# Kernel tuning notes

Measured on AMD Instinct MI355X. Metric: run time of the kernel, lower is better.

## Reference

```python
import jax, jax.numpy as jnp
import numpy as np
from jax.scipy.linalg import solve_triangular

EPS = 2e-05  # module eps (original only adds it on Cholesky failure)
NUM_LABELS = 8


def setup_inputs() -> dict:
    key = jax.random.key(0)
    k1, k2, k3, k4 = jax.random.split(key, 4)
    B, N, H, W = 1, 256, 512, 512
    return {
        "content_feat": jax.random.normal(k1, (B, N, H, W), dtype=jnp.float32),
        "style_feat": jax.random.normal(k2, (B, N, H, W), dtype=jnp.float32),
        "content_seg": jax.random.randint(k3, (H, W), 0, NUM_LABELS, dtype=jnp.int32),
        "style_seg": jax.random.randint(k4, (H, W), 0, NUM_LABELS, dtype=jnp.int32),
        "num_labels": NUM_LABELS,
    }


def _cwct(c, s, seg_c, seg_s, num_labels):
    # c, s: (N, M) flattened features; seg_*: (M,) int labels
    N = c.shape[0]
    eye = jnp.eye(N, dtype=c.dtype)
    target = c
    for l in range(num_labels):  # fixed small label count
        mc = (seg_c == l)  # (Mc,) content mask
        ms = (seg_s == l)
        nc = mc.sum().astype(c.dtype)
        ns = ms.sum().astype(c.dtype)
        nc1 = jnp.maximum(nc, 1.0)
        ns1 = jnp.maximum(ns, 1.0)
        # masked mean + centered (zeros outside mask)
        mean_c = (c * mc).sum(-1) / nc1
        xc = (c - mean_c[:, None]) * mc  # (N, M)
        cov_c = (xc @ xc.T) / jnp.maximum(nc1 - 1.0, 1.0)  # (N, N)
        Lc = jnp.linalg.cholesky(cov_c)
        inv_Lc = solve_triangular(Lc, eye, lower=True)
        white = inv_Lc @ xc
        # style stats + coloring
        mean_s = (s * ms).sum(-1) / ns1
        xs = (s - mean_s[:, None]) * ms
        cov_s = (xs @ xs.T) / jnp.maximum(ns1 - 1.0, 1.0)
        Ls = jnp.linalg.cholesky(cov_s)
        colored = Ls @ white + mean_s[:, None]
        # label validity: >10 pixels each side, count ratio < 100
        valid = (nc > 10) & (ns > 10) & (nc < 100.0 * ns) & (ns < 100.0 * nc)
        target = jnp.where(mc[None, :] & valid, colored, target)
    return target


def reference(content_feat, style_feat, content_seg, style_seg, num_labels):
    B, N, cH, cW = content_feat.shape  # B == 1 (original code only supports B=1)
    c = content_feat.reshape(N, cH * cW)
    s = style_feat.reshape(N, -1)
    out = _cwct(c, s, content_seg.reshape(-1), style_seg.reshape(-1), num_labels)
    return out.reshape(B, N, cH, cW)
```

## Files before the change

kernel.cpp:

```cpp
#include <hip/hip_runtime.h>

#define NCH   256
#define M_PIX 262144
#define MPAD  266240
#define LDA   40

typedef short bf16x8 __attribute__((ext_vector_type(8)));
typedef float f32x4  __attribute__((ext_vector_type(4)));

__device__ __forceinline__ unsigned short f2bf(float f) {
  union { float f; unsigned u; } v; v.f = f;
  unsigned r = v.u + 0x7FFFu + ((v.u >> 16) & 1u);
  return (unsigned short)(r >> 16);
}
__device__ __forceinline__ float bf2f(unsigned short h) {
  union { unsigned u; float f; } v; v.u = ((unsigned)h) << 16;
  return v.f;
}

__global__ __launch_bounds__(256) void k_hist(const int* __restrict__ seg_c,
                                              const int* __restrict__ seg_s,
                                              int* __restrict__ hist) {
  __shared__ int h[16];
  int t = threadIdx.x;
  if (t < 16) h[t] = 0;
  __syncthreads();
  int p0 = blockIdx.x * 2048 + t * 8;
#pragma unroll
  for (int e = 0; e < 8; ++e) {
    atomicAdd(&h[seg_c[p0 + e] & 7], 1);
    atomicAdd(&h[8 + (seg_s[p0 + e] & 7)], 1);
  }
  __syncthreads();
  if (t < 8) hist[blockIdx.x * 8 + t] = h[t];
  else if (t < 16) hist[1024 + blockIdx.x * 8 + (t - 8)] = h[t];
}

__global__ __launch_bounds__(256) void k_scan(const int* __restrict__ hist,
                                              int* __restrict__ base,
                                              int* __restrict__ off,
                                              int* __restrict__ cnt,
                                              int* __restrict__ valid) {
  __shared__ int lh[2048];
  __shared__ int tot[16];
  __shared__ int loff[2][9];
  int t = threadIdx.x;
  for (int i = t; i < 2048; i += 256) lh[i] = hist[i];
  __syncthreads();
  if (t < 16) {
    int s = t >> 3, l = t & 7, acc = 0;
    for (int b = 0; b < 128; ++b) acc += lh[s * 1024 + b * 8 + l];
    tot[t] = acc;
  }
  __syncthreads();
  if (t < 2) {
    int run = 0;
    for (int l = 0; l < 8; ++l) {
      loff[t][l] = run;
      run = (run + tot[t * 8 + l] + 511) & ~511;
    }
    loff[t][8] = run;
    for (int l = 0; l < 9; ++l) off[t * 9 + l] = loff[t][l];
    for (int l = 0; l < 8; ++l) cnt[t * 8 + l] = tot[t * 8 + l];
  }
  __syncthreads();
  if (t < 8) {
    long nc = tot[t], ns = tot[8 + t];
    valid[t] = (nc > 10 && ns > 10 && nc < 100 * ns && ns < 100 * nc) ? 1 : 0;
  }
  if (t < 16) {
    int s = t >> 3, l = t & 7;
    int run = loff[s][l];
    for (int b = 0; b < 128; ++b) {
      base[s * 1024 + b * 8 + l] = run;
      run += lh[s * 1024 + b * 8 + l];
    }
  }
}

__global__ __launch_bounds__(256) void k_rank(const int* __restrict__ seg_c,
                                              const int* __restrict__ seg_s,
                                              const int* __restrict__ base,
                                              int* __restrict__ dst) {
  __shared__ int sc[8 * 272];
  __shared__ int rb[256 * 8];
  __shared__ int bb[8];
  int t = threadIdx.x;
  for (int s = 0; s < 2; ++s) {
    const int* seg = s ? seg_s : seg_c;
    const int* bas = base + s * 1024 + blockIdx.x * 8;
    int* dd = dst + (size_t)s * M_PIX;
    int p0 = blockIdx.x * 2048 + t * 8;
    unsigned pk2 = 0, cpk = 0;
#pragma unroll
    for (int e = 0; e < 8; ++e) {
      int lb = seg[p0 + e] & 7;
      pk2 |= (unsigned)lb << (3 * e);
      cpk += 1u << (4 * lb);
    }
#pragma unroll
    for (int lq = 0; lq < 8; ++lq) sc[lq * 272 + t] = (int)((cpk >> (4 * lq)) & 15u);
    if (t < 8) bb[t] = bas[t];
    __syncthreads();
    for (int d = 1; d < 256; d <<= 1) {
      int v[8];
#pragma unroll
      for (int lq = 0; lq < 8; ++lq)
        v[lq] = sc[lq * 272 + t] + ((t >= d) ? sc[lq * 272 + t - d] : 0);
      __syncthreads();
#pragma unroll
      for (int lq = 0; lq < 8; ++lq) sc[lq * 272 + t] = v[lq];
      __syncthreads();
    }
#pragma unroll
    for (int lq = 0; lq < 8; ++lq)
      rb[t * 8 + lq] = bb[lq] + sc[lq * 272 + t] - (int)((cpk >> (4 * lq)) & 15u);
#pragma unroll
    for (int e = 0; e < 8; ++e) {
      int lb = (int)((pk2 >> (3 * e)) & 7u);
      int dpos = rb[t * 8 + lb]++;
      dd[p0 + e] = dpos;
    }
    __syncthreads();
  }
}

__global__ __launch_bounds__(256) void k_padzero(unsigned short* __restrict__ P,
                                                 const int* __restrict__ off,
                                                 const int* __restrict__ cnt) {
  int l = blockIdx.x;
  int c0, c1;
  if (l < 8) { c0 = off[l] + cnt[l]; c1 = off[l + 1]; }
  else       { c0 = off[8];          c1 = MPAD; }
  int w = c1 - c0;
  if (w <= 0) return;
  for (int r = 0; r < 256; ++r)
    for (int cc = threadIdx.x; cc < w; cc += 256)
      P[(size_t)r * MPAD + c0 + cc] = 0;
}

__global__ __launch_bounds__(256) void k_pack(const float* __restrict__ feat,
                                              const int* __restrict__ seg,
                                              const int* __restrict__ dst,
                                              const int* __restrict__ base,
                                              unsigned short* __restrict__ P) {
  int b = blockIdx.x, g = blockIdx.y, t = threadIdx.x;
  int p0 = b * 2048;
  __shared__ unsigned short buf[8][2048];
  __shared__ int h[8], lbase[9], gbase[8];
  if (t < 8) { h[t] = 0; gbase[t] = base[b * 8 + t]; }
  __syncthreads();
  int lb[8], slot[8], gd[8];
#pragma unroll
  for (int i = 0; i < 8; ++i) {
    lb[i] = seg[p0 + i * 256 + t] & 7;
    atomicAdd(&h[lb[i]], 1);
  }
  __syncthreads();
  if (t == 0) {
    int run = 0;
    for (int l = 0; l < 8; ++l) { lbase[l] = run; run += h[l]; }
    lbase[8] = run;
  }
  __syncthreads();
#pragma unroll
  for (int i = 0; i < 8; ++i)
    slot[i] = lbase[lb[i]] + (dst[p0 + i * 256 + t] - gbase[lb[i]]);
#pragma unroll
  for (int i = 0; i < 8; ++i) {
    int q = i * 256 + t;
    int l = 0;
    while (l < 7 && q >= lbase[l + 1]) ++l;
    gd[i] = gbase[l] + q - lbase[l];
  }
  int n0 = g * 32;
#pragma unroll 1
  for (int cp = 0; cp < 4; ++cp) {
#pragma unroll
    for (int c = 0; c < 8; ++c) {
      const float* fp = &feat[(size_t)(n0 + cp * 8 + c) * M_PIX + p0];
#pragma unroll
      for (int i = 0; i < 8; ++i)
        buf[c][slot[i]] = f2bf(fp[i * 256 + t]);
    }
    __syncthreads();
#pragma unroll
    for (int c = 0; c < 8; ++c) {
      unsigned short* pp = &P[(size_t)(n0 + cp * 8 + c) * MPAD];
#pragma unroll
      for (int i = 0; i < 8; ++i)
        pp[gd[i]] = buf[c][i * 256 + t];
    }
    __syncthreads();
  }
}

__global__ __launch_bounds__(256) void k_unpack(const unsigned short* __restrict__ P,
                                                const int* __restrict__ seg,
                                                const int* __restrict__ dst,
                                                const int* __restrict__ base,
                                                float* __restrict__ out) {
  int b = blockIdx.x, g = blockIdx.y, t = threadIdx.x;
  int p0 = b * 2048;
  __shared__ unsigned short buf[8][2048];
  __shared__ int h[8], lbase[9], gbase[8];
  if (t < 8) { h[t] = 0; gbase[t] = base[b * 8 + t]; }
  __syncthreads();
  int lb[8], slot[8], gd[8];
#pragma unroll
  for (int i = 0; i < 8; ++i) {
    lb[i] = seg[p0 + i * 256 + t] & 7;
    atomicAdd(&h[lb[i]], 1);
  }
  __syncthreads();
  if (t == 0) {
    int run = 0;
    for (int l = 0; l < 8; ++l) { lbase[l] = run; run += h[l]; }
    lbase[8] = run;
  }
  __syncthreads();
#pragma unroll
  for (int i = 0; i < 8; ++i)
    slot[i] = lbase[lb[i]] + (dst[p0 + i * 256 + t] - gbase[lb[i]]);
#pragma unroll
  for (int i = 0; i < 8; ++i) {
    int q = i * 256 + t;
    int l = 0;
    while (l < 7 && q >= lbase[l + 1]) ++l;
    gd[i] = gbase[l] + q - lbase[l];
  }
  int n0 = g * 32;
#pragma unroll 1
  for (int cp = 0; cp < 4; ++cp) {
#pragma unroll
    for (int c = 0; c < 8; ++c) {
      const unsigned short* pp = &P[(size_t)(n0 + cp * 8 + c) * MPAD];
#pragma unroll
      for (int i = 0; i < 8; ++i)
        buf[c][i * 256 + t] = pp[gd[i]];
    }
    __syncthreads();
#pragma unroll
    for (int c = 0; c < 8; ++c) {
      float* op = &out[(size_t)(n0 + cp * 8 + c) * M_PIX + p0];
#pragma unroll
      for (int i = 0; i < 8; ++i)
        op[i * 256 + t] = bf2f(buf[c][slot[i]]);
    }
    __syncthreads();
  }
}

__global__ __launch_bounds__(512) void k_gram(const unsigned short* __restrict__ P,
                                              const int* __restrict__ off,
                                              float* __restrict__ G,
                                              float* __restrict__ sum) {
  int l = blockIdx.y;
  long o0 = off[l], o1 = off[l + 1];
  long k0 = o0 + (long)blockIdx.x * 1024;
  if (k0 >= o1) return;
  long rem = o1 - k0;
  int ks = rem > 1024 ? 1024 : (int)rem;

  __shared__ unsigned short Sb[256 * LDA];
  int t = threadIdx.x, wave = t >> 6, lane = t & 63;
  int wr = (wave < 2) ? wave * 64 : 128 + (wave & 1) * 64;
  int wc = (wave >= 4) ? 128 : 0;
  bool wact = (wave < 6);

  f32x4 acc[4][8] = {};
  float rsum = 0.0f;

  for (int kk = 0; kk < ks; kk += 32) {
#pragma unroll
    for (int it = 0; it < 2; ++it) {
      int slot = t + it * 512;
      int rr = slot >> 2, gg = slot & 3;
      *(uint4*)&Sb[rr * LDA + gg * 8] =
          *(const uint4*)&P[(size_t)rr * MPAD + (size_t)(k0 + kk) + gg * 8];
    }
    __syncthreads();
    if (t < 256) {
#pragma unroll
      for (int e = 0; e < 16; ++e) {
        unsigned v = *(const unsigned*)&Sb[t * LDA + e * 2];
        rsum += bf2f((unsigned short)(v & 0xFFFFu)) + bf2f((unsigned short)(v >> 16));
      }
    }
    if (wact) {
      bf16x8 bfr[8];
#pragma unroll
      for (int fj = 0; fj < 8; ++fj)
        bfr[fj] = *(const bf16x8*)&Sb[(wc + fj * 16 + (lane & 15)) * LDA + (lane >> 4) * 8];
#pragma unroll
      for (int fi = 0; fi < 4; ++fi) {
        bf16x8 afr = *(const bf16x8*)&Sb[(wr + fi * 16 + (lane & 15)) * LDA + (lane >> 4) * 8];
#pragma unroll
        for (int fj = 0; fj < 8; ++fj)
          acc[fi][fj] = __builtin_amdgcn_mfma_f32_16x16x32_bf16(afr, bfr[fj], acc[fi][fj], 0, 0, 0);
      }
    }
    __syncthreads();
  }
  float* Gl = G + ((size_t)l << 16);
  if (wact) {
#pragma unroll
    for (int fi = 0; fi < 4; ++fi)
#pragma unroll
      for (int fj = 0; fj < 8; ++fj) {
        int cc = wc + fj * 16 + (lane & 15);
#pragma unroll
        for (int rg = 0; rg < 4; ++rg) {
          int rr2 = wr + fi * 16 + (lane >> 4) * 4 + rg;
          atomicAdd(&Gl[rr2 * 256 + cc], acc[fi][fj][rg]);
        }
      }
  }
  if (t < 256) atomicAdd(&sum[l * 256 + t], rsum);
}

__global__ __launch_bounds__(256) void k_cov(float* __restrict__ G,
                                             const float* __restrict__ sum,
                                             const int* __restrict__ cnt,
                                             float* __restrict__ means) {
  int bid = blockIdx.x;
  float* A = G + ((size_t)bid << 16);
  int t = threadIdx.x;
  __shared__ float mu[256];
  float fc = (float)cnt[bid];
  float m = sum[bid * 256 + t] / fmaxf(fc, 1.0f);
  mu[t] = m;
  means[bid * 256 + t] = m;
  __syncthreads();
  float rdiv = 1.0f / fmaxf(fmaxf(fc, 1.0f) - 1.0f, 1.0f);
  float mt = mu[t];
  for (int i = t; i < 256; ++i) {
    float g = A[i * 256 + t];
    A[t * 256 + i] = (g - fc * mu[i] * mt) * rdiv;
  }
}

__global__ __launch_bounds__(256) void k_panel(float* __restrict__ G,
                                               float* __restrict__ Wg,
                                               int pb) {
  float* LT = G + ((size_t)blockIdx.x << 16);
  int t = threadIdx.x;
  int jbase = pb * 32;
  int H2 = 224 - jbase;
  __shared__ float Wl[32 * 36];

  if (t < 64) {
    int l32 = t & 31;
    float x[32];
#pragma unroll
    for (int k = 0; k < 32; ++k)
      x[k] = (k <= l32) ? LT[(size_t)(jbase + k) * 256 + jbase + l32] : 0.0f;
#pragma unroll
    for (int j = 0; j < 32; ++j) {
      float dj = __shfl(x[j], j, 64);
      float rd = 1.0f / sqrtf(dj);
      float lj = x[j] * rd;
      x[j] = lj;
#pragma unroll
      for (int k = j + 1; k < 32; ++k) {
        float lkj = __shfl(lj, k, 64);
        x[k] -= lj * lkj;
      }
    }
    if (t < 32) {
#pragma unroll
      for (int k = 0; k < 32; ++k)
        if (k <= l32) LT[(size_t)(jbase + k) * 256 + jbase + l32] = x[k];
    }
    float w[32];
#pragma unroll
    for (int k = 0; k < 32; ++k) w[k] = 0.0f;
#pragma unroll
    for (int i2 = 0; i2 < 32; ++i2) {
      float s = (i2 == l32) ? 1.0f : 0.0f;
#pragma unroll
      for (int k = 0; k < 32; ++k)
        if (k < i2) s -= __shfl(x[k], i2, 64) * w[k];
      float Lii = __shfl(x[i2], i2, 64);
      float wv = s / Lii;
      w[i2] = (i2 >= l32) ? wv : 0.0f;
    }
    if (t < 32) {
      float* Wgp = Wg + (((size_t)blockIdx.x * 8 + pb) << 10);
#pragma unroll
      for (int i2 = 0; i2 < 32; ++i2)
        if (i2 >= l32) {
          Wl[i2 * 36 + l32] = w[i2];
          Wgp[i2 * 32 + l32] = w[i2];
        }
    }
  }
  __syncthreads();

  if (t < H2) {
    int r = jbase + 32 + t;
    float a[32];
#pragma unroll
    for (int k = 0; k < 32; ++k) a[k] = LT[(size_t)(jbase + k) * 256 + r];
#pragma unroll
    for (int j = 0; j < 32; ++j) {
      float s = 0.0f;
#pragma unroll
      for (int k = 0; k < 32; ++k)
        if (k <= j) s += a[k] * Wl[j * 36 + k];
      LT[(size_t)(jbase + j) * 256 + r] = s;
    }
  }
}

__global__ __launch_bounds__(256) void k_trail(float* __restrict__ G, int pb) {
  int jbase = pb * 32;
  int H2 = 224 - jbase;
  int nts2 = (H2 + 63) >> 6;
  int y = blockIdx.y;
  if (y >= (nts2 * (nts2 + 1)) >> 1) return;
  int ti = 0;
  while ((((ti + 1) * (ti + 2)) >> 1) <= y) ++ti;
  int tj = y - ((ti * (ti + 1)) >> 1);
  float* LT = G + ((size_t)blockIdx.x << 16);
  int i0 = jbase + 32 + ti * 64;
  int j0 = jbase + 32 + tj * 64;

  __shared__ float Li[32][64];
  __shared__ float Lj[32][64];
  int t = threadIdx.x;
  for (int idx = t; idx < 2048; idx += 256) {
    int k = idx >> 6, r = idx & 63;
    Li[k][r] = (i0 + r < 256) ? LT[(size_t)(jbase + k) * 256 + i0 + r] : 0.0f;
    Lj[k][r] = (j0 + r < 256) ? LT[(size_t)(jbase + k) * 256 + j0 + r] : 0.0f;
  }
  __syncthreads();

  int tx = t & 15, ty = t >> 4;
  float acc[4][4] = {};
#pragma unroll
  for (int k = 0; k < 32; ++k) {
    float4 a = *(const float4*)&Li[k][ty * 4];
    float4 b = *(const float4*)&Lj[k][tx * 4];
    acc[0][0] += a.x * b.x; acc[0][1] += a.x * b.y; acc[0][2] += a.x * b.z; acc[0][3] += a.x * b.w;
    acc[1][0] += a.y * b.x; acc[1][1] += a.y * b.y; acc[1][2] += a.y * b.z; acc[1][3] += a.y * b.w;
    acc[2][0] += a.z * b.x; acc[2][1] += a.z * b.y; acc[2][2] += a.z * b.z; acc[2][3] += a.z * b.w;
    acc[3][0] += a.w * b.x; acc[3][1] += a.w * b.y; acc[3][2] += a.w * b.z; acc[3][3] += a.w * b.w;
  }
#pragma unroll
  for (int jj = 0; jj < 4; ++jj) {
    int j = j0 + tx * 4 + jj;
    if (j >= 256) continue;
    float* col = &LT[(size_t)j * 256 + i0 + ty * 4];
#pragma unroll
    for (int ii = 0; ii < 4; ++ii) {
      int i = i0 + ty * 4 + ii;
      if (i < 256 && i >= j) col[ii] -= acc[ii][jj];
    }
  }
}

__global__ __launch_bounds__(256) void k_vinit(const float* __restrict__ Wg,
                                               float* __restrict__ Vinv) {
  int l = blockIdx.x;
  float* V = Vinv + ((size_t)l << 16);
  const float* W = Wg + ((size_t)l * 8) * 1024;
  int t = threadIdx.x;
  for (int pb = 0; pb < 8; ++pb)
    for (int idx = t; idx < 1024; idx += 256) {
      int i = idx >> 5, j = idx & 31;
      V[(size_t)(pb * 32 + i) * 256 + pb * 32 + j] = (i >= j) ? W[pb * 1024 + idx] : 0.0f;
    }
}

template <int N>
__global__ __launch_bounds__(512) void k_vlevel(const float* __restrict__ G,
                                                float* __restrict__ Vinv) {
  constexpr int NP = 256 / (2 * N);
  constexpr int RPT = N / 32;
  constexpr int CPT = N / 16;
  int unit = blockIdx.x;
  int l = unit / NP, pair = unit % NP;
  const float* LT = G + ((size_t)l << 16);
  float* V = Vinv + ((size_t)l << 16);
  int d = pair * 2 * N;
  int t = threadIdx.x;
  int cg = t & 15, rg = t >> 4;
  int r0 = rg * RPT, c0 = cg * CPT;

  __shared__ float Abuf[N][N + 4];
  __shared__ float Bbuf[N][N + 4];

  for (int idx = t; idx < N * N; idx += 512) {
    int k = idx / N, r = idx % N;
    Abuf[r][k] = LT[(size_t)(d + k) * 256 + d + N + r];
  }
  for (int idx = t; idx < N * N; idx += 512) {
    int k = idx / N, c = idx % N;
    Bbuf[k][c] = V[(size_t)(d + k) * 256 + d + c];
  }
  __syncthreads();

  float acc[RPT][CPT];
#pragma unroll
  for (int i = 0; i < RPT; ++i)
#pragma unroll
    for (int j = 0; j < CPT; ++j) acc[i][j] = 0.0f;
  for (int k = 0; k < N; ++k) {
    float av[RPT];
#pragma unroll
    for (int i = 0; i < RPT; ++i) av[i] = Abuf[r0 + i][k];
#pragma unroll
    for (int j = 0; j < CPT; ++j) {
      float bv = Bbuf[k][c0 + j];
#pragma unroll
      for (int i = 0; i < RPT; ++i) acc[i][j] += av[i] * bv;
    }
  }
  __syncthreads();
#pragma unroll
  for (int i = 0; i < RPT; ++i)
#pragma unroll
    for (int j = 0; j < CPT; ++j) Abuf[r0 + i][c0 + j] = acc[i][j];
  for (int idx = t; idx < N * N; idx += 512) {
    int r = idx / N, k = idx % N;
    Bbuf[r][k] = V[(size_t)(d + N + r) * 256 + d + N + k];
  }
  __syncthreads();

#pragma unroll
  for (int i = 0; i < RPT; ++i)
#pragma unroll
    for (int j = 0; j < CPT; ++j) acc[i][j] = 0.0f;
  for (int k = 0; k < N; ++k) {
    float av[RPT];
#pragma unroll
    for (int i = 0; i < RPT; ++i) av[i] = Bbuf[r0 + i][k];
#pragma unroll
    for (int j = 0; j < CPT; ++j) {
      float bv = Abuf[k][c0 + j];
#pragma unroll
      for (int i = 0; i < RPT; ++i) acc[i][j] += av[i] * bv;
    }
  }
#pragma unroll
  for (int i = 0; i < RPT; ++i)
#pragma unroll
    for (int j = 0; j < CPT; ++j)
      V[(size_t)(d + N + r0 + i) * 256 + d + c0 + j] = -acc[i][j];
}

__global__ __launch_bounds__(256) void k_tgemm(const float* __restrict__ G,
                                               const float* __restrict__ Vinv,
                                               const float* __restrict__ means,
                                               const int* __restrict__ valid,
                                               unsigned short* __restrict__ Tb,
                                               float* __restrict__ bacc) {
  int l = blockIdx.y;
  int ti = blockIdx.x >> 2, tj = blockIdx.x & 3;
  unsigned short* Tbl = Tb + ((size_t)l << 16);
  int i0 = ti * 64, j0 = tj * 64;
  int t = threadIdx.x;
  if (!valid[l]) {
    for (int idx = t; idx < 4096; idx += 256) {
      int i = idx >> 6, j = idx & 63;
      Tbl[(size_t)(i0 + i) * 256 + j0 + j] = f2bf((i0 + i) == (j0 + j) ? 1.0f : 0.0f);
    }
    return;
  }
  if (tj > ti) {
    for (int idx = t; idx < 4096; idx += 256) {
      int i = idx >> 6, j = idx & 63;
      Tbl[(size_t)(i0 + i) * 256 + j0 + j] = 0;
    }
    return;
  }
  const float* LTs = G + ((size_t)(8 + l) << 16);
  const float* V = Vinv + ((size_t)l << 16);

  __shared__ float As[64][260];
  __shared__ __align__(16) float Bs[256][68];

  for (int idx = t; idx < 64 * 256; idx += 256) {
    int k = idx >> 6, i = idx & 63;
    As[i][k] = (i0 + i >= k) ? LTs[(size_t)k * 256 + i0 + i] : 0.0f;
  }
  for (int idx = t; idx < 64 * 256; idx += 256) {
    int k = idx >> 6, j = idx & 63;
    Bs[k][j] = V[(size_t)k * 256 + j0 + j];
  }
  __syncthreads();

  int tx = t & 15, ty = t >> 4;
  float acc[4][4] = {};
  int klo = j0, khi = i0 + 64;
  for (int k = klo; k < khi; ++k) {
    float a0 = As[ty * 4 + 0][k], a1 = As[ty * 4 + 1][k];
    float a2 = As[ty * 4 + 2][k], a3 = As[ty * 4 + 3][k];
    float4 b = *(const float4*)&Bs[k][tx * 4];
    acc[0][0] += a0 * b.x; acc[0][1] += a0 * b.y; acc[0][2] += a0 * b.z; acc[0][3] += a0 * b.w;
    acc[1][0] += a1 * b.x; acc[1][1] += a1 * b.y; acc[1][2] += a1 * b.z; acc[1][3] += a1 * b.w;
    acc[2][0] += a2 * b.x; acc[2][1] += a2 * b.y; acc[2][2] += a2 * b.z; acc[2][3] += a2 * b.w;
    acc[3][0] += a3 * b.x; acc[3][1] += a3 * b.y; acc[3][2] += a3 * b.z; acc[3][3] += a3 * b.w;
  }
  float mc[4];
#pragma unroll
  for (int cc = 0; cc < 4; ++cc) mc[cc] = means[l * 256 + j0 + tx * 4 + cc];
#pragma unroll
  for (int rr = 0; rr < 4; ++rr) {
    int i = i0 + ty * 4 + rr;
    float partial = 0.0f;
#pragma unroll
    for (int cc = 0; cc < 4; ++cc) {
      Tbl[(size_t)i * 256 + j0 + tx * 4 + cc] = f2bf(acc[rr][cc]);
      partial += acc[rr][cc] * mc[cc];
    }
    atomicAdd(&bacc[l * 256 + i], partial);
  }
}

__global__ __launch_bounds__(256) void k_bvec(const float* __restrict__ means,
                                              const float* __restrict__ bacc,
                                              const int* __restrict__ valid,
                                              float* __restrict__ bvec) {
  int l = blockIdx.x, i = threadIdx.x;
  bvec[l * 256 + i] = valid[l] ? (means[(8 + l) * 256 + i] - bacc[l * 256 + i]) : 0.0f;
}

__global__ __launch_bounds__(256) void k_outgemm(unsigned short* __restrict__ P,
                                                 const unsigned short* __restrict__ Tb,
                                                 const float* __restrict__ bvec,
                                                 const int* __restrict__ off) {
  long px0 = (long)blockIdx.x * 128;
  if (px0 >= off[8]) return;
  int l = 0;
  while (l < 7 && px0 >= off[l + 1]) ++l;
  const unsigned short* Tl = Tb + ((size_t)l << 16);

  __shared__ unsigned short As[256 * LDA];
  __shared__ unsigned short Bs[128 * LDA];
  __shared__ float bsh[256];

  int t = threadIdx.x, wave = t >> 6, lane = t & 63;
  int wrow = wave * 64;
  bsh[t] = bvec[l * 256 + t];

  f32x4 acc[4][8] = {};

  for (int kk = 0; kk < 256; kk += 32) {
#pragma unroll
    for (int it = 0; it < 4; ++it) {
      int slot = t + it * 256;
      int rr = slot >> 2, gg = slot & 3;
      *(uint4*)&As[rr * LDA + gg * 8] = *(const uint4*)&Tl[rr * 256 + kk + gg * 8];
    }
#pragma unroll
    for (int it = 0; it < 2; ++it) {
      int slot = t + it * 256;
      int pg = slot & 15, kr = slot >> 4;
      uint4 v = *(const uint4*)&P[(size_t)(kk + kr) * MPAD + px0 + pg * 8];
      const unsigned short* vs = (const unsigned short*)&v;
      int krs = kr ^ ((pg & 3) << 3);
#pragma unroll
      for (int e = 0; e < 8; ++e) Bs[(pg * 8 + e) * LDA + krs] = vs[e];
    }
    __syncthreads();
    if (kk < wrow + 64) {
      bf16x8 bfr[8];
#pragma unroll
      for (int fj = 0; fj < 8; ++fj) {
        int px = fj * 16 + (lane & 15);
        int gs = (lane >> 4) ^ ((px >> 3) & 3);
        bfr[fj] = *(const bf16x8*)&Bs[px * LDA + gs * 8];
      }
#pragma unroll
      for (int fi = 0; fi < 4; ++fi) {
        if (wrow + fi * 16 + 15 >= kk) {
          bf16x8 afr = *(const bf16x8*)&As[(wrow + fi * 16 + (lane & 15)) * LDA + (lane >> 4) * 8];
#pragma unroll
          for (int fj = 0; fj < 8; ++fj)
            acc[fi][fj] = __builtin_amdgcn_mfma_f32_16x16x32_bf16(afr, bfr[fj], acc[fi][fj], 0, 0, 0);
        }
      }
    }
    __syncthreads();
  }
#pragma unroll
  for (int fi = 0; fi < 4; ++fi)
#pragma unroll
    for (int fj = 0; fj < 8; ++fj) {
      long p = px0 + fj * 16 + (lane & 15);
#pragma unroll
      for (int rg = 0; rg < 4; ++rg) {
        int rr = wrow + fi * 16 + (lane >> 4) * 4 + rg;
        float v = acc[fi][fj][rg] + bsh[rr];
        P[(size_t)rr * MPAD + p] = f2bf(v);
      }
    }
}

extern "C" void kernel_launch(void* const* d_in, const int* in_sizes, int n_in,
                              void* d_out, int out_size, void* d_ws, size_t ws_size,
                              hipStream_t stream) {
  const float* cfeat = (const float*)d_in[0];
  const float* sfeat = (const float*)d_in[1];
  const int* seg_c   = (const int*)d_in[2];
  const int* seg_s   = (const int*)d_in[3];

  char* ws = (char*)d_ws;
  size_t o = 0;
  auto take = [&](size_t b) { size_t r = o; o += (b + 255) & ~(size_t)255; return r; };

  unsigned short* P  = (unsigned short*)(ws + take((size_t)NCH * MPAD * 2));
  size_t zero_b = o;
  float* G           = (float*)(ws + take((size_t)2 * 8 * 65536 * 4));
  float* Vinv        = (float*)(ws + take((size_t)8 * 65536 * 4));
  float* sum         = (float*)(ws + take((size_t)2 * 8 * 256 * 4));
  float* bacc        = (float*)(ws + take((size_t)8 * 256 * 4));
  int*   hist        = (int*)(ws + take((size_t)2 * 128 * 8 * 4));
  size_t zero_e = o;
  unsigned short* Tb = (unsigned short*)(ws + take((size_t)8 * 65536 * 2));
  float* Wg          = (float*)(ws + take((size_t)16 * 8 * 1024 * 4));
  int*   dst         = (int*)(ws + take((size_t)2 * M_PIX * 4));
  float* means       = (float*)(ws + take((size_t)2 * 8 * 256 * 4));
  float* bvec        = (float*)(ws + take((size_t)8 * 256 * 4));
  int*   base        = (int*)(ws + take((size_t)2 * 128 * 8 * 4));
  int*   off         = (int*)(ws + take((size_t)2 * 9 * 4));
  int*   cnt         = (int*)(ws + take((size_t)2 * 8 * 4));
  int*   valid       = (int*)(ws + take((size_t)8 * 4));
  (void)ws_size; (void)n_in; (void)in_sizes; (void)out_size;

  hipMemsetAsync(ws + zero_b, 0, zero_e - zero_b, stream);

  k_hist<<<dim3(128), dim3(256), 0, stream>>>(seg_c, seg_s, hist);
  k_scan<<<dim3(1), dim3(256), 0, stream>>>(hist, base, off, cnt, valid);
  k_rank<<<dim3(128), dim3(256), 0, stream>>>(seg_c, seg_s, base, dst);

  for (int s = 1; s >= 0; --s) {
    const float* feat = s ? sfeat : cfeat;
    const int* seg = s ? seg_s : seg_c;
    k_padzero<<<dim3(9), dim3(256), 0, stream>>>(P, off + s * 9, cnt + s * 8);
    k_pack<<<dim3(128, 8), dim3(256), 0, stream>>>(feat, seg, dst + (size_t)s * M_PIX,
                                                   base + s * 1024, P);
    k_gram<<<dim3(260, 8), dim3(512), 0, stream>>>(P, off + s * 9, G + (size_t)s * 8 * 65536,
                                                   sum + (size_t)s * 8 * 256);
  }

  k_cov<<<dim3(16), dim3(256), 0, stream>>>(G, sum, cnt, means);
  for (int pb = 0; pb < 8; ++pb) {
    k_panel<<<dim3(16), dim3(256), 0, stream>>>(G, Wg, pb);
    if (pb < 7) k_trail<<<dim3(16, 10), dim3(256), 0, stream>>>(G, pb);
  }
  k_vinit<<<dim3(8), dim3(256), 0, stream>>>(Wg, Vinv);
  k_vlevel<32><<<dim3(32), dim3(512), 0, stream>>>(G, Vinv);
  k_vlevel<64><<<dim3(16), dim3(512), 0, stream>>>(G, Vinv);
  k_vlevel<128><<<dim3(8), dim3(512), 0, stream>>>(G, Vinv);
  k_tgemm<<<dim3(16, 8), dim3(256), 0, stream>>>(G, Vinv, means, valid, Tb, bacc);
  k_bvec<<<dim3(8), dim3(256), 0, stream>>>(means, bacc, valid, bvec);
  k_outgemm<<<dim3(2080), dim3(256), 0, stream>>>(P, Tb, bvec, off);
  k_unpack<<<dim3(128, 8), dim3(256), 0, stream>>>(P, seg_c, dst, base, (float*)d_out);
}
```

Baseline: 1.144 ms.

## Use 64-wide Cholesky panels and fuse small kernels to cut launches

The blocked Cholesky now works on 64-column panels. Each panel kernel factors two 32-blocks and applies the intra-panel update itself, which halves the panel/trailing launch sequence. The V-inverse init and first level merge into one kernel that builds the 64x64 diagonal inverses. The bias is now accumulated straight into bacc, seeded with the style means, which drops the k_bvec kernel. This reduces the many small serial launches in the tiny factorization phase, at the cost of more per-thread serial work inside each panel kernel.

```diff
diff --git a/kernel.cpp b/kernel.cpp
--- a/kernel.cpp
+++ b/kernel.cpp
@@ -322,7 +322,8 @@
 __global__ __launch_bounds__(256) void k_cov(float* __restrict__ G,
                                              const float* __restrict__ sum,
                                              const int* __restrict__ cnt,
-                                             float* __restrict__ means) {
+                                             float* __restrict__ means,
+                                             float* __restrict__ bacc) {
   int bid = blockIdx.x;
   float* A = G + ((size_t)bid << 16);
   int t = threadIdx.x;
@@ -331,6 +332,7 @@
   float m = sum[bid * 256 + t] / fmaxf(fc, 1.0f);
   mu[t] = m;
   means[bid * 256 + t] = m;
+  if (bid >= 8) bacc[(bid - 8) * 256 + t] = m;
   __syncthreads();
   float rdiv = 1.0f / fmaxf(fmaxf(fc, 1.0f) - 1.0f, 1.0f);
   float mt = mu[t];
@@ -340,21 +342,23 @@
   }
 }
 
-__global__ __launch_bounds__(256) void k_panel(float* __restrict__ G,
-                                               float* __restrict__ Wg,
-                                               int pb) {
+__global__ __launch_bounds__(256) void k_panel64(float* __restrict__ G,
+                                                 float* __restrict__ Wg, int pb) {
   float* LT = G + ((size_t)blockIdx.x << 16);
   int t = threadIdx.x;
-  int jbase = pb * 32;
-  int H2 = 224 - jbase;
-  __shared__ float Wl[32 * 36];
+  int jb = pb * 64;
+  int nT = 224 - jb;
+  __shared__ float W1[32 * 36];
+  __shared__ float W2[32 * 36];
+  __shared__ float Cb[32][33];
+  __shared__ float Db[32][33];
 
   if (t < 64) {
     int l32 = t & 31;
     float x[32];
 #pragma unroll
     for (int k = 0; k < 32; ++k)
-      x[k] = (k <= l32) ? LT[(size_t)(jbase + k) * 256 + jbase + l32] : 0.0f;
+      x[k] = (k <= l32) ? LT[(size_t)(jb + k) * 256 + jb + l32] : 0.0f;
 #pragma unroll
     for (int j = 0; j < 32; ++j) {
       float dj = __shfl(x[j], j, 64);
@@ -362,15 +366,13 @@
       float lj = x[j] * rd;
       x[j] = lj;
 #pragma unroll
-      for (int k = j + 1; k < 32; ++k) {
-        float lkj = __shfl(lj, k, 64);
-        x[k] -= lj * lkj;
-      }
+      for (int k = j + 1; k < 32; ++k)
+        x[k] -= lj * __shfl(lj, k, 64);
     }
     if (t < 32) {
 #pragma unroll
       for (int k = 0; k < 32; ++k)
-        if (k <= l32) LT[(size_t)(jbase + k) * 256 + jbase + l32] = x[k];
+        if (k <= l32) LT[(size_t)(jb + k) * 256 + jb + l32] = x[k];
     }
     float w[32];
 #pragma unroll
@@ -381,65 +383,136 @@
 #pragma unroll
       for (int k = 0; k < 32; ++k)
         if (k < i2) s -= __shfl(x[k], i2, 64) * w[k];
-      float Lii = __shfl(x[i2], i2, 64);
-      float wv = s / Lii;
+      float wv = s / __shfl(x[i2], i2, 64);
       w[i2] = (i2 >= l32) ? wv : 0.0f;
     }
     if (t < 32) {
-      float* Wgp = Wg + (((size_t)blockIdx.x * 8 + pb) << 10);
+      float* Wgp = Wg + (((size_t)blockIdx.x * 8 + 2 * pb) << 10);
 #pragma unroll
       for (int i2 = 0; i2 < 32; ++i2)
-        if (i2 >= l32) {
-          Wl[i2 * 36 + l32] = w[i2];
-          Wgp[i2 * 32 + l32] = w[i2];
-        }
-    }
-  }
-  __syncthreads();
-
-  if (t < H2) {
-    int r = jbase + 32 + t;
+        if (i2 >= l32) { W1[i2 * 36 + l32] = w[i2]; Wgp[i2 * 32 + l32] = w[i2]; }
+    }
+  }
+  __syncthreads();
+
+  float xx[32], bb[32];
+  if (t < nT) {
+    int row = jb + 32 + t;
     float a[32];
 #pragma unroll
-    for (int k = 0; k < 32; ++k) a[k] = LT[(size_t)(jbase + k) * 256 + r];
+    for (int k = 0; k < 32; ++k) a[k] = LT[(size_t)(jb + k) * 256 + row];
 #pragma unroll
     for (int j = 0; j < 32; ++j) {
       float s = 0.0f;
 #pragma unroll
       for (int k = 0; k < 32; ++k)
-        if (k <= j) s += a[k] * Wl[j * 36 + k];
-      LT[(size_t)(jbase + j) * 256 + r] = s;
-    }
-  }
-}
-
-__global__ __launch_bounds__(256) void k_trail(float* __restrict__ G, int pb) {
-  int jbase = pb * 32;
-  int H2 = 224 - jbase;
-  int nts2 = (H2 + 63) >> 6;
+        if (k <= j) s += a[k] * W1[j * 36 + k];
+      xx[j] = s;
+      LT[(size_t)(jb + j) * 256 + row] = s;
+    }
+    if (t < 32) {
+#pragma unroll
+      for (int j = 0; j < 32; ++j) Cb[t][j] = xx[j];
+    }
+  }
+  __syncthreads();
+
+  if (t < nT) {
+    int row = jb + 32 + t;
+#pragma unroll
+    for (int c = 0; c < 32; ++c) {
+      float s = LT[(size_t)(jb + 32 + c) * 256 + row];
+#pragma unroll
+      for (int k = 0; k < 32; ++k) s -= xx[k] * Cb[c][k];
+      bb[c] = s;
+    }
+    if (t < 32) {
+#pragma unroll
+      for (int c = 0; c < 32; ++c) Db[t][c] = bb[c];
+    }
+  }
+  __syncthreads();
+
+  if (t < 64) {
+    int l32 = t & 31;
+    float x[32];
+#pragma unroll
+    for (int k = 0; k < 32; ++k) x[k] = (k <= l32) ? Db[l32][k] : 0.0f;
+#pragma unroll
+    for (int j = 0; j < 32; ++j) {
+      float dj = __shfl(x[j], j, 64);
+      float rd = 1.0f / sqrtf(dj);
+      float lj = x[j] * rd;
+      x[j] = lj;
+#pragma unroll
+      for (int k = j + 1; k < 32; ++k)
+        x[k] -= lj * __shfl(lj, k, 64);
+    }
+    if (t < 32) {
+#pragma unroll
+      for (int k = 0; k < 32; ++k)
+        if (k <= l32) LT[(size_t)(jb + 32 + k) * 256 + jb + 32 + l32] = x[k];
+    }
+    float w[32];
+#pragma unroll
+    for (int k = 0; k < 32; ++k) w[k] = 0.0f;
+#pragma unroll
+    for (int i2 = 0; i2 < 32; ++i2) {
+      float s = (i2 == l32) ? 1.0f : 0.0f;
+#pragma unroll
+      for (int k = 0; k < 32; ++k)
+        if (k < i2) s -= __shfl(x[k], i2, 64) * w[k];
+      float wv = s / __shfl(x[i2], i2, 64);
+      w[i2] = (i2 >= l32) ? wv : 0.0f;
+    }
+    if (t < 32) {
+      float* Wgp = Wg + (((size_t)blockIdx.x * 8 + 2 * pb + 1) << 10);
+#pragma unroll
+      for (int i2 = 0; i2 < 32; ++i2)
+        if (i2 >= l32) { W2[i2 * 36 + l32] = w[i2]; Wgp[i2 * 32 + l32] = w[i2]; }
+    }
+  }
+  __syncthreads();
+
+  if (t >= 32 && t < nT) {
+    int row = jb + 32 + t;
+#pragma unroll
+    for (int j = 0; j < 32; ++j) {
+      float s = 0.0f;
+#pragma unroll
+      for (int k = 0; k < 32; ++k)
+        if (k <= j) s += bb[k] * W2[j * 36 + k];
+      LT[(size_t)(jb + 32 + j) * 256 + row] = s;
+    }
+  }
+}
+
+__global__ __launch_bounds__(256) void k_trail64(float* __restrict__ G, int pb) {
+  int jb = pb * 64;
+  int H2 = 192 - jb;
+  int nts2 = H2 >> 6;
   int y = blockIdx.y;
   if (y >= (nts2 * (nts2 + 1)) >> 1) return;
   int ti = 0;
   while ((((ti + 1) * (ti + 2)) >> 1) <= y) ++ti;
   int tj = y - ((ti * (ti + 1)) >> 1);
   float* LT = G + ((size_t)blockIdx.x << 16);
-  int i0 = jbase + 32 + ti * 64;
-  int j0 = jbase + 32 + tj * 64;
-
-  __shared__ float Li[32][64];
-  __shared__ float Lj[32][64];
+  int i0 = jb + 64 + ti * 64, j0 = jb + 64 + tj * 64;
+
+  __shared__ float Li[64][64];
+  __shared__ float Lj[64][64];
   int t = threadIdx.x;
-  for (int idx = t; idx < 2048; idx += 256) {
+  for (int idx = t; idx < 4096; idx += 256) {
     int k = idx >> 6, r = idx & 63;
-    Li[k][r] = (i0 + r < 256) ? LT[(size_t)(jbase + k) * 256 + i0 + r] : 0.0f;
-    Lj[k][r] = (j0 + r < 256) ? LT[(size_t)(jbase + k) * 256 + j0 + r] : 0.0f;
+    Li[k][r] = LT[(size_t)(jb + k) * 256 + i0 + r];
+    Lj[k][r] = LT[(size_t)(jb + k) * 256 + j0 + r];
   }
   __syncthreads();
 
   int tx = t & 15, ty = t >> 4;
   float acc[4][4] = {};
-#pragma unroll
-  for (int k = 0; k < 32; ++k) {
+#pragma unroll 4
+  for (int k = 0; k < 64; ++k) {
     float4 a = *(const float4*)&Li[k][ty * 4];
     float4 b = *(const float4*)&Lj[k][tx * 4];
     acc[0][0] += a.x * b.x; acc[0][1] += a.x * b.y; acc[0][2] += a.x * b.z; acc[0][3] += a.x * b.w;
@@ -450,27 +523,58 @@
 #pragma unroll
   for (int jj = 0; jj < 4; ++jj) {
     int j = j0 + tx * 4 + jj;
-    if (j >= 256) continue;
     float* col = &LT[(size_t)j * 256 + i0 + ty * 4];
 #pragma unroll
     for (int ii = 0; ii < 4; ++ii) {
       int i = i0 + ty * 4 + ii;
-      if (i < 256 && i >= j) col[ii] -= acc[ii][jj];
-    }
-  }
-}
-
-__global__ __launch_bounds__(256) void k_vinit(const float* __restrict__ Wg,
-                                               float* __restrict__ Vinv) {
-  int l = blockIdx.x;
+      if (i >= j) col[ii] -= acc[ii][jj];
+    }
+  }
+}
+
+__global__ __launch_bounds__(256) void k_vlevel32w(const float* __restrict__ G,
+                                                   const float* __restrict__ Wg,
+                                                   float* __restrict__ Vinv) {
+  int l = blockIdx.x >> 2, pair = blockIdx.x & 3;
+  const float* LT = G + ((size_t)l << 16);
   float* V = Vinv + ((size_t)l << 16);
-  const float* W = Wg + ((size_t)l * 8) * 1024;
+  const float* W1g = Wg + (((size_t)l * 8 + 2 * pair) << 10);
+  const float* W2g = Wg + (((size_t)l * 8 + 2 * pair + 1) << 10);
+  int d = pair * 64;
   int t = threadIdx.x;
-  for (int pb = 0; pb < 8; ++pb)
-    for (int idx = t; idx < 1024; idx += 256) {
-      int i = idx >> 5, j = idx & 31;
-      V[(size_t)(pb * 32 + i) * 256 + pb * 32 + j] = (i >= j) ? W[pb * 1024 + idx] : 0.0f;
-    }
+  __shared__ float A[32][33];
+  __shared__ float B[32][33];
+  __shared__ float C[32][33];
+  for (int idx = t; idx < 1024; idx += 256) {
+    int i = idx >> 5, j = idx & 31;
+    A[i][j] = LT[(size_t)(d + j) * 256 + d + 32 + i];
+    float w1 = (i >= j) ? W1g[idx] : 0.0f;
+    B[i][j] = w1;
+    V[(size_t)(d + i) * 256 + d + j] = w1;
+  }
+  __syncthreads();
+  for (int idx = t; idx < 1024; idx += 256) {
+    int i = idx >> 5, j = idx & 31;
+    float s = 0.0f;
+#pragma unroll
+    for (int k = 0; k < 32; ++k) s += A[i][k] * B[k][j];
+    C[i][j] = s;
+  }
+  __syncthreads();
+  for (int idx = t; idx < 1024; idx += 256) {
+    int i = idx >> 5, j = idx & 31;
+    float w2 = (i >= j) ? W2g[idx] : 0.0f;
+    B[i][j] = w2;
+    V[(size_t)(d + 32 + i) * 256 + d + 32 + j] = w2;
+  }
+  __syncthreads();
+  for (int idx = t; idx < 1024; idx += 256) {
+    int i = idx >> 5, j = idx & 31;
+    float s = 0.0f;
+#pragma unroll
+    for (int k = 0; k < 32; ++k) s += B[i][k] * C[k][j];
+    V[(size_t)(d + 32 + i) * 256 + d + j] = -s;
+  }
 }
 
 template <int N>
@@ -562,6 +666,7 @@
   int i0 = ti * 64, j0 = tj * 64;
   int t = threadIdx.x;
   if (!valid[l]) {
+    if (tj == 0 && t < 64) bacc[l * 256 + i0 + t] = 0.0f;
     for (int idx = t; idx < 4096; idx += 256) {
       int i = idx >> 6, j = idx & 63;
       Tbl[(size_t)(i0 + i) * 256 + j0 + j] = f2bf((i0 + i) == (j0 + j) ? 1.0f : 0.0f);
@@ -615,16 +720,8 @@
       Tbl[(size_t)i * 256 + j0 + tx * 4 + cc] = f2bf(acc[rr][cc]);
       partial += acc[rr][cc] * mc[cc];
     }
-    atomicAdd(&bacc[l * 256 + i], partial);
-  }
-}
-
-__global__ __launch_bounds__(256) void k_bvec(const float* __restrict__ means,
-                                              const float* __restrict__ bacc,
-                                              const int* __restrict__ valid,
-                                              float* __restrict__ bvec) {
-  int l = blockIdx.x, i = threadIdx.x;
-  bvec[l * 256 + i] = valid[l] ? (means[(8 + l) * 256 + i] - bacc[l * 256 + i]) : 0.0f;
+    atomicAdd(&bacc[l * 256 + i], -partial);
+  }
 }
 
 __global__ __launch_bounds__(256) void k_outgemm(unsigned short* __restrict__ P,
@@ -723,7 +820,6 @@
   float* Wg          = (float*)(ws + take((size_t)16 * 8 * 1024 * 4));
   int*   dst         = (int*)(ws + take((size_t)2 * M_PIX * 4));
   float* means       = (float*)(ws + take((size_t)2 * 8 * 256 * 4));
-  float* bvec        = (float*)(ws + take((size_t)8 * 256 * 4));
   int*   base        = (int*)(ws + take((size_t)2 * 128 * 8 * 4));
   int*   off         = (int*)(ws + take((size_t)2 * 9 * 4));
   int*   cnt         = (int*)(ws + take((size_t)2 * 8 * 4));
@@ -746,17 +842,18 @@
                                                    sum + (size_t)s * 8 * 256);
   }
 
-  k_cov<<<dim3(16), dim3(256), 0, stream>>>(G, sum, cnt, means);
-  for (int pb = 0; pb < 8; ++pb) {
-    k_panel<<<dim3(16), dim3(256), 0, stream>>>(G, Wg, pb);
-    if (pb < 7) k_trail<<<dim3(16, 10), dim3(256), 0, stream>>>(G, pb);
-  }
-  k_vinit<<<dim3(8), dim3(256), 0, stream>>>(Wg, Vinv);
-  k_vlevel<32><<<dim3(32), dim3(512), 0, stream>>>(G, Vinv);
+  k_cov<<<dim3(16), dim3(256), 0, stream>>>(G, sum, cnt, means, bacc);
+  for (int pb = 0; pb < 4; ++pb) {
+    k_panel64<<<dim3(16), dim3(256), 0, stream>>>(G, Wg, pb);
+    if (pb < 3) {
+      int nts2 = (192 - 64 * pb) >> 6;
+      k_trail64<<<dim3(16, (nts2 * (nts2 + 1)) >> 1), dim3(256), 0, stream>>>(G, pb);
+    }
+  }
+  k_vlevel32w<<<dim3(32), dim3(256), 0, stream>>>(G, Wg, Vinv);
   k_vlevel<64><<<dim3(16), dim3(512), 0, stream>>>(G, Vinv);
   k_vlevel<128><<<dim3(8), dim3(512), 0, stream>>>(G, Vinv);
   k_tgemm<<<dim3(16, 8), dim3(256), 0, stream>>>(G, Vinv, means, valid, Tb, bacc);
-  k_bvec<<<dim3(8), dim3(256), 0, stream>>>(means, bacc, valid, bvec);
-  k_outgemm<<<dim3(2080), dim3(256), 0, stream>>>(P, Tb, bvec, off);
+  k_outgemm<<<dim3(2080), dim3(256), 0, stream>>>(P, Tb, bacc, off);
   k_unpack<<<dim3(128, 8), dim3(256), 0, stream>>>(P, seg_c, dst, base, (float*)d_out);
 }
```

Result: no change. 1.145 ms (+0.1%).
